# Kernel tuning notes

Measured on AMD Instinct MI355X. Metric: run time of the kernel, lower is better.

Reference implementation:

```python
import jax, jax.numpy as jnp
import numpy as np

MUL = 128          # multiplicity for every irrep
N = 100000         # number of nodes
INV_SQRT_FANIN = 1.0 / np.sqrt(MUL).astype(np.float32)


def setup_inputs() -> dict:
    key = jax.random.key(0)
    k = jax.random.split(key, 5)
    return {
        "x": jax.random.normal(k[0], (N, MUL + 3 * MUL), dtype=jnp.float32),   # [N, 512] = 128x0e + 128x1o
        "w1_s": jax.random.normal(k[1], (MUL, 2 * MUL), dtype=jnp.float32),    # 0e path of linear_1 (-> scalars+gates)
        "w1_v": jax.random.normal(k[2], (MUL, MUL), dtype=jnp.float32),        # 1o path of linear_1
        "w2_s": jax.random.normal(k[3], (MUL, MUL), dtype=jnp.float32),        # 0e path of linear_2
        "w2_v": jax.random.normal(k[4], (MUL, MUL), dtype=jnp.float32),        # 1o path of linear_2
    }


def reference(x, w1_s, w1_v, w2_s, w2_v):
    n = x.shape[0]
    x0 = x[:, :MUL]                              # [N, 128]  scalars (0e)
    x1 = x[:, MUL:].reshape(n, MUL, 3)           # [N, 128, 3] vectors (1o)

    # linear_1: 128x0e+128x1o -> 256x0e + 128x1o (scalars | gates | gated)
    s = (x0 @ w1_s) * INV_SQRT_FANIN             # [N, 256]
    v = jnp.einsum('nui,uv->nvi', x1, w1_v) * INV_SQRT_FANIN  # [N, 128, 3]

    # Gate: silu on scalars, silu(gates) broadcast-multiplies the vectors
    h0 = jax.nn.silu(s[:, :MUL])                 # [N, 128]
    g = jax.nn.silu(s[:, MUL:])                  # [N, 128]
    h1 = v * g[:, :, None]                       # [N, 128, 3]

    # linear_2: 128x0e+128x1o -> 128x0e+128x1o
    y0 = (h0 @ w2_s) * INV_SQRT_FANIN            # [N, 128]
    y1 = jnp.einsum('nui,uv->nvi', h1, w2_v) * INV_SQRT_FANIN  # [N, 128, 3]
    return jnp.concatenate([y0, y1.reshape(n, 3 * MUL)], axis=-1)  # [N, 512]
```

## Files before the change

### kernel.cpp

```cpp
#include <hip/hip_runtime.h>
#include <hip/hip_bf16.h>
#include <cstdint>

#define MUL   128
#define ROWS  32
#define NW    8
#define TPB   (NW * 64)

typedef __attribute__((ext_vector_type(8))) short  short8;
typedef __attribute__((ext_vector_type(8))) __bf16 bf16x8;
typedef __attribute__((ext_vector_type(4))) float  f32x4;
typedef __attribute__((ext_vector_type(4))) short  short4v;

__device__ __forceinline__ short f2bf(float f) {
    union { float f; unsigned int u; } v; v.f = f;
    unsigned int u = v.u;
    u += 0x7fffu + ((u >> 16) & 1u);
    return (short)(u >> 16);
}

__device__ __forceinline__ float silu_f(float x) {
    return x / (1.0f + __expf(-x));
}

#define RSB     256
#define OFF_X0  0
#define OFF_X1  8192
#define OFF_H0  32768
#define OFF_H1  40960
#define SMEM_BYTES 65536

__device__ __forceinline__ int swz(int row, int byteInRow) {
    return row * RSB + (byteInRow ^ ((row & 7) << 4));
}

__device__ __forceinline__ short8 lds_afrag(const char* sm, int off, int r0, int ks, int lane) {
    int row = r0 + (lane & 15);
    int bi  = ks * 64 + ((lane >> 4) << 4);
    return *(const short8*)(sm + off + swz(row, bi));
}

__device__ __forceinline__ short8 bfrag_f32(const float* __restrict__ W, int ldn,
                                            int c0, int ks, int lane) {
    const float* p = W + (size_t)(ks * 32 + ((lane >> 4) << 3)) * ldn + (c0 + (lane & 15));
    short8 r;
#pragma unroll
    for (int j = 0; j < 8; ++j) r[j] = f2bf(p[(size_t)j * ldn]);
    return r;
}

__device__ __forceinline__ f32x4 mfma16(short8 a, short8 b, f32x4 c) {
    return __builtin_amdgcn_mfma_f32_16x16x32_bf16(
        __builtin_bit_cast(bf16x8, a), __builtin_bit_cast(bf16x8, b), c, 0, 0, 0);
}

__global__ __launch_bounds__(TPB, 4) void gnlr_fused_kernel(
    const float* __restrict__ x,
    const float* __restrict__ w1s, const float* __restrict__ w1v,
    const float* __restrict__ w2s, const float* __restrict__ w2v,
    float* __restrict__ out, int n)
{
    __shared__ alignas(16) char sm[SMEM_BYTES];

    const int tid   = threadIdx.x;
    const int lane  = tid & 63;
    const int w     = tid >> 6;
    const int row0g = blockIdx.x * ROWS;
    const float INV = 0.08838834764831845f;

#pragma unroll
    for (int it = 0; it < 2; ++it) {
        int idx = tid + it * TPB;
        int row = idx >> 5;
        int c4  = (idx & 31) << 2;
        int rg  = row0g + row; if (rg >= n) rg = n - 1;
        float4 f = *(const float4*)(x + (size_t)rg * 512 + c4);
        short4v pk;
        pk.x = f2bf(f.x); pk.y = f2bf(f.y); pk.z = f2bf(f.z); pk.w = f2bf(f.w);
        *(short4v*)(sm + OFF_X0 + swz(row, c4 * 2)) = pk;
    }
#pragma unroll
    for (int it = 0; it < 2; ++it) {
        int idx = tid + it * TPB;
        int row = idx >> 5;
        int grp = idx & 31;
        int rg  = row0g + row; if (rg >= n) rg = n - 1;
        const float* p = x + (size_t)rg * 512 + 128 + grp * 12;
        float4 fa = *(const float4*)(p);
        float4 fb = *(const float4*)(p + 4);
        float4 fc = *(const float4*)(p + 8);
        float f[12] = { fa.x, fa.y, fa.z, fa.w, fb.x, fb.y, fb.z, fb.w, fc.x, fc.y, fc.z, fc.w };
#pragma unroll
        for (int i = 0; i < 3; ++i) {
            short4v pk;
            pk.x = f2bf(f[i]); pk.y = f2bf(f[3 + i]); pk.z = f2bf(f[6 + i]); pk.w = f2bf(f[9 + i]);
            *(short4v*)(sm + OFF_X1 + i * 8192 + swz(row, grp * 8)) = pk;
        }
    }
    __syncthreads();

    const f32x4 z = { 0.f, 0.f, 0.f, 0.f };
    const int c0 = w * 16;

    short8 bs0[4], bs1[4];
#pragma unroll
    for (int ks = 0; ks < 4; ++ks) {
        bs0[ks] = bfrag_f32(w1s, 256, c0, ks, lane);
        bs1[ks] = bfrag_f32(w1s, 256, 128 + c0, ks, lane);
    }
    float g_reg[2][4];
#pragma unroll
    for (int rt = 0; rt < 2; ++rt) {
        f32x4 a0 = z, a1 = z;
#pragma unroll
        for (int ks = 0; ks < 4; ++ks) {
            short8 a = lds_afrag(sm, OFF_X0, rt * 16, ks, lane);
            a0 = mfma16(a, bs0[ks], a0);
            a1 = mfma16(a, bs1[ks], a1);
        }
#pragma unroll
        for (int j = 0; j < 4; ++j) {
            int row = rt * 16 + ((lane >> 4) << 2) + j;
            int col = c0 + (lane & 15);
            float h0 = silu_f(a0[j] * INV);
            *(short*)(sm + OFF_H0 + swz(row, col * 2)) = f2bf(h0);
            g_reg[rt][j] = silu_f(a1[j] * INV);
        }
    }

    short8 bv[4];
#pragma unroll
    for (int ks = 0; ks < 4; ++ks) bv[ks] = bfrag_f32(w1v, 128, c0, ks, lane);
#pragma unroll
    for (int i = 0; i < 3; ++i) {
#pragma unroll
        for (int rt = 0; rt < 2; ++rt) {
            f32x4 acc = z;
#pragma unroll
            for (int ks = 0; ks < 4; ++ks) {
                short8 a = lds_afrag(sm, OFF_X1 + i * 8192, rt * 16, ks, lane);
                acc = mfma16(a, bv[ks], acc);
            }
#pragma unroll
            for (int j = 0; j < 4; ++j) {
                int row = rt * 16 + ((lane >> 4) << 2) + j;
                int col = c0 + (lane & 15);
                float h1 = acc[j] * INV * g_reg[rt][j];
                *(short*)(sm + OFF_H1 + i * 8192 + swz(row, col * 2)) = f2bf(h1);
            }
        }
    }
    __syncthreads();

    short8 b2s[4], b2v[4];
#pragma unroll
    for (int ks = 0; ks < 4; ++ks) {
        b2s[ks] = bfrag_f32(w2s, 128, c0, ks, lane);
        b2v[ks] = bfrag_f32(w2v, 128, c0, ks, lane);
    }
#pragma unroll
    for (int rt = 0; rt < 2; ++rt) {
        f32x4 acc = z;
#pragma unroll
        for (int ks = 0; ks < 4; ++ks)
            acc = mfma16(lds_afrag(sm, OFF_H0, rt * 16, ks, lane), b2s[ks], acc);
#pragma unroll
        for (int j = 0; j < 4; ++j) {
            int row = rt * 16 + ((lane >> 4) << 2) + j;
            int rg  = row0g + row;
            if (rg < n) out[(size_t)rg * 512 + c0 + (lane & 15)] = acc[j] * INV;
        }
    }
#pragma unroll
    for (int i = 0; i < 3; ++i) {
#pragma unroll
        for (int rt = 0; rt < 2; ++rt) {
            f32x4 acc = z;
#pragma unroll
            for (int ks = 0; ks < 4; ++ks)
                acc = mfma16(lds_afrag(sm, OFF_H1 + i * 8192, rt * 16, ks, lane), b2v[ks], acc);
#pragma unroll
            for (int j = 0; j < 4; ++j) {
                int row = rt * 16 + ((lane >> 4) << 2) + j;
                int rg  = row0g + row;
                if (rg < n) out[(size_t)rg * 512 + 128 + 3 * (c0 + (lane & 15)) + i] = acc[j] * INV;
            }
        }
    }
}

extern "C" void kernel_launch(void* const* d_in, const int* in_sizes, int n_in,
                              void* d_out, int out_size, void* d_ws, size_t ws_size,
                              hipStream_t stream) {
    const float* x   = (const float*)d_in[0];
    const float* w1s = (const float*)d_in[1];
    const float* w1v = (const float*)d_in[2];
    const float* w2s = (const float*)d_in[3];
    const float* w2v = (const float*)d_in[4];
    float* out = (float*)d_out;
    const int n = in_sizes[0] / (4 * MUL);
    const int grid = (n + ROWS - 1) / ROWS;
    gnlr_fused_kernel<<<grid, TPB, 0, stream>>>(x, w1s, w1v, w2s, w2v, out, n);
}
```

Before: 127.3 us.

## Prepack bf16 weight fragments, swap MFMA operands, reuse LDS, vectorize stores

A small prep kernel converts all four weight matrices once into bf16 MFMA fragment layout in workspace, so each block loads a packed fragment with one coalesced load instead of eight strided fp32 loads and conversions. The MFMA operands are swapped so each lane holds four consecutive columns of one row, which allows float4 output stores and interleaves the three vector components into contiguous stores. The gated-vector intermediate now overwrites the x0/x1 regions of shared memory, shrinking LDS to 40KB to allow 8 blocks per CU, at the cost of extra barriers per component. An extra kernel launch is added per call.

```diff
diff --git a/kernel.cpp b/kernel.cpp
--- a/kernel.cpp
+++ b/kernel.cpp
@@ -1,11 +1,8 @@
 #include <hip/hip_runtime.h>
-#include <hip/hip_bf16.h>
 #include <cstdint>
 
-#define MUL   128
-#define ROWS  32
-#define NW    8
-#define TPB   (NW * 64)
+#define TPB  512
+#define ROWS 32
 
 typedef __attribute__((ext_vector_type(8))) short  short8;
 typedef __attribute__((ext_vector_type(8))) __bf16 bf16x8;
@@ -18,35 +15,34 @@
     u += 0x7fffu + ((u >> 16) & 1u);
     return (short)(u >> 16);
 }
-
-__device__ __forceinline__ float silu_f(float x) {
-    return x / (1.0f + __expf(-x));
-}
-
-#define RSB     256
-#define OFF_X0  0
-#define OFF_X1  8192
-#define OFF_H0  32768
-#define OFF_H1  40960
-#define SMEM_BYTES 65536
-
-__device__ __forceinline__ int swz(int row, int byteInRow) {
-    return row * RSB + (byteInRow ^ ((row & 7) << 4));
-}
-
-__device__ __forceinline__ short8 lds_afrag(const char* sm, int off, int r0, int ks, int lane) {
+__device__ __forceinline__ float silu_f(float x) { return x / (1.0f + __expf(-x)); }
+
+#define RSB 256
+#define OFF_X0 0
+#define OFF_X1 8192
+#define OFF_H0 32768
+#define SMEM_BYTES 40960
+
+__device__ __forceinline__ int swz(int row, int b) { return row * RSB + (b ^ ((row & 7) << 4)); }
+
+__device__ __forceinline__ short8 lds_bfrag(const char* sm, int off, int r0, int ks, int lane) {
     int row = r0 + (lane & 15);
     int bi  = ks * 64 + ((lane >> 4) << 4);
     return *(const short8*)(sm + off + swz(row, bi));
 }
 
-__device__ __forceinline__ short8 bfrag_f32(const float* __restrict__ W, int ldn,
-                                            int c0, int ks, int lane) {
-    const float* p = W + (size_t)(ks * 32 + ((lane >> 4) << 3)) * ldn + (c0 + (lane & 15));
-    short8 r;
-#pragma unroll
-    for (int j = 0; j < 8; ++j) r[j] = f2bf(p[(size_t)j * ldn]);
-    return r;
+template<bool PACKED>
+__device__ __forceinline__ short8 wfrag(const short8* pw, const float* W, int ldn,
+                                        int gtile, int ltile, int ks, int lane) {
+    if constexpr (PACKED) {
+        return pw[(gtile * 4 + ks) * 64 + lane];
+    } else {
+        const float* p = W + (size_t)(ks * 32 + ((lane >> 4) << 3)) * ldn + ltile * 16 + (lane & 15);
+        short8 r;
+#pragma unroll
+        for (int j = 0; j < 8; ++j) r[j] = f2bf(p[(size_t)j * ldn]);
+        return r;
+    }
 }
 
 __device__ __forceinline__ f32x4 mfma16(short8 a, short8 b, f32x4 c) {
@@ -54,10 +50,30 @@
         __builtin_bit_cast(bf16x8, a), __builtin_bit_cast(bf16x8, b), c, 0, 0, 0);
 }
 
-__global__ __launch_bounds__(TPB, 4) void gnlr_fused_kernel(
+__global__ void prep_pack(const float* __restrict__ w1s, const float* __restrict__ w1v,
+                          const float* __restrict__ w2s, const float* __restrict__ w2v,
+                          short8* __restrict__ pk) {
+    int b = blockIdx.x;
+    int t = threadIdx.x;
+    int ks = t >> 6, lane = t & 63;
+    const float* W; int ldn, lt;
+    if (b < 16)      { W = w1s; ldn = 256; lt = b; }
+    else if (b < 24) { W = w1v; ldn = 128; lt = b - 16; }
+    else if (b < 32) { W = w2s; ldn = 128; lt = b - 24; }
+    else             { W = w2v; ldn = 128; lt = b - 32; }
+    const float* p = W + (size_t)(ks * 32 + ((lane >> 4) << 3)) * ldn + lt * 16 + (lane & 15);
+    short8 r;
+#pragma unroll
+    for (int j = 0; j < 8; ++j) r[j] = f2bf(p[(size_t)j * ldn]);
+    pk[(b * 4 + ks) * 64 + lane] = r;
+}
+
+template<bool PACKED>
+__global__ __launch_bounds__(TPB, 8) void gnlr_fused_kernel(
     const float* __restrict__ x,
     const float* __restrict__ w1s, const float* __restrict__ w1v,
     const float* __restrict__ w2s, const float* __restrict__ w2v,
+    const short8* __restrict__ pw,
     float* __restrict__ out, int n)
 {
     __shared__ alignas(16) char sm[SMEM_BYTES];
@@ -66,7 +82,9 @@
     const int lane  = tid & 63;
     const int w     = tid >> 6;
     const int row0g = blockIdx.x * ROWS;
+    const int c0    = w * 16;
     const float INV = 0.08838834764831845f;
+    const f32x4 z = { 0.f, 0.f, 0.f, 0.f };
 
 #pragma unroll
     for (int it = 0; it < 2; ++it) {
@@ -75,9 +93,9 @@
         int c4  = (idx & 31) << 2;
         int rg  = row0g + row; if (rg >= n) rg = n - 1;
         float4 f = *(const float4*)(x + (size_t)rg * 512 + c4);
-        short4v pk;
-        pk.x = f2bf(f.x); pk.y = f2bf(f.y); pk.z = f2bf(f.z); pk.w = f2bf(f.w);
-        *(short4v*)(sm + OFF_X0 + swz(row, c4 * 2)) = pk;
+        short4v pkv;
+        pkv.x = f2bf(f.x); pkv.y = f2bf(f.y); pkv.z = f2bf(f.z); pkv.w = f2bf(f.w);
+        *(short4v*)(sm + OFF_X0 + swz(row, c4 * 2)) = pkv;
     }
 #pragma unroll
     for (int it = 0; it < 2; ++it) {
@@ -92,98 +110,103 @@
         float f[12] = { fa.x, fa.y, fa.z, fa.w, fb.x, fb.y, fb.z, fb.w, fc.x, fc.y, fc.z, fc.w };
 #pragma unroll
         for (int i = 0; i < 3; ++i) {
-            short4v pk;
-            pk.x = f2bf(f[i]); pk.y = f2bf(f[3 + i]); pk.z = f2bf(f[6 + i]); pk.w = f2bf(f[9 + i]);
-            *(short4v*)(sm + OFF_X1 + i * 8192 + swz(row, grp * 8)) = pk;
+            short4v pkv;
+            pkv.x = f2bf(f[i]); pkv.y = f2bf(f[3 + i]); pkv.z = f2bf(f[6 + i]); pkv.w = f2bf(f[9 + i]);
+            *(short4v*)(sm + OFF_X1 + i * 8192 + swz(row, grp * 8)) = pkv;
         }
     }
     __syncthreads();
 
-    const f32x4 z = { 0.f, 0.f, 0.f, 0.f };
-    const int c0 = w * 16;
-
-    short8 bs0[4], bs1[4];
-#pragma unroll
-    for (int ks = 0; ks < 4; ++ks) {
-        bs0[ks] = bfrag_f32(w1s, 256, c0, ks, lane);
-        bs1[ks] = bfrag_f32(w1s, 256, 128 + c0, ks, lane);
-    }
     float g_reg[2][4];
-#pragma unroll
-    for (int rt = 0; rt < 2; ++rt) {
-        f32x4 a0 = z, a1 = z;
-#pragma unroll
-        for (int ks = 0; ks < 4; ++ks) {
-            short8 a = lds_afrag(sm, OFF_X0, rt * 16, ks, lane);
-            a0 = mfma16(a, bs0[ks], a0);
-            a1 = mfma16(a, bs1[ks], a1);
-        }
-#pragma unroll
-        for (int j = 0; j < 4; ++j) {
-            int row = rt * 16 + ((lane >> 4) << 2) + j;
-            int col = c0 + (lane & 15);
-            float h0 = silu_f(a0[j] * INV);
-            *(short*)(sm + OFF_H0 + swz(row, col * 2)) = f2bf(h0);
-            g_reg[rt][j] = silu_f(a1[j] * INV);
-        }
-    }
-
-    short8 bv[4];
-#pragma unroll
-    for (int ks = 0; ks < 4; ++ks) bv[ks] = bfrag_f32(w1v, 128, c0, ks, lane);
-#pragma unroll
-    for (int i = 0; i < 3; ++i) {
+    {
+        short8 bs[4];
+#pragma unroll
+        for (int ks = 0; ks < 4; ++ks) bs[ks] = wfrag<PACKED>(pw, w1s, 256, w, w, ks, lane);
 #pragma unroll
         for (int rt = 0; rt < 2; ++rt) {
             f32x4 acc = z;
 #pragma unroll
-            for (int ks = 0; ks < 4; ++ks) {
-                short8 a = lds_afrag(sm, OFF_X1 + i * 8192, rt * 16, ks, lane);
-                acc = mfma16(a, bv[ks], acc);
-            }
-#pragma unroll
-            for (int j = 0; j < 4; ++j) {
-                int row = rt * 16 + ((lane >> 4) << 2) + j;
-                int col = c0 + (lane & 15);
-                float h1 = acc[j] * INV * g_reg[rt][j];
-                *(short*)(sm + OFF_H1 + i * 8192 + swz(row, col * 2)) = f2bf(h1);
+            for (int ks = 0; ks < 4; ++ks)
+                acc = mfma16(bs[ks], lds_bfrag(sm, OFF_X0, rt * 16, ks, lane), acc);
+            short4v pkv;
+#pragma unroll
+            for (int j = 0; j < 4; ++j) pkv[j] = f2bf(silu_f(acc[j] * INV));
+            int row = rt * 16 + (lane & 15);
+            *(short4v*)(sm + OFF_H0 + swz(row, 2 * (c0 + ((lane >> 4) << 2)))) = pkv;
+        }
+#pragma unroll
+        for (int ks = 0; ks < 4; ++ks) bs[ks] = wfrag<PACKED>(pw, w1s, 256, 8 + w, 8 + w, ks, lane);
+#pragma unroll
+        for (int rt = 0; rt < 2; ++rt) {
+            f32x4 acc = z;
+#pragma unroll
+            for (int ks = 0; ks < 4; ++ks)
+                acc = mfma16(bs[ks], lds_bfrag(sm, OFF_X0, rt * 16, ks, lane), acc);
+#pragma unroll
+            for (int j = 0; j < 4; ++j) g_reg[rt][j] = silu_f(acc[j] * INV);
+        }
+    }
+
+    {
+        short8 bv[4];
+#pragma unroll
+        for (int ks = 0; ks < 4; ++ks) bv[ks] = wfrag<PACKED>(pw, w1v, 128, 16 + w, w, ks, lane);
+#pragma unroll
+        for (int i = 0; i < 3; ++i) {
+            __syncthreads();
+#pragma unroll
+            for (int rt = 0; rt < 2; ++rt) {
+                f32x4 acc = z;
+#pragma unroll
+                for (int ks = 0; ks < 4; ++ks)
+                    acc = mfma16(bv[ks], lds_bfrag(sm, OFF_X1 + i * 8192, rt * 16, ks, lane), acc);
+                short4v pkv;
+#pragma unroll
+                for (int j = 0; j < 4; ++j) pkv[j] = f2bf(acc[j] * INV * g_reg[rt][j]);
+                int row = rt * 16 + (lane & 15);
+                *(short4v*)(sm + i * 8192 + swz(row, 2 * (c0 + ((lane >> 4) << 2)))) = pkv;
             }
         }
     }
     __syncthreads();
 
-    short8 b2s[4], b2v[4];
-#pragma unroll
-    for (int ks = 0; ks < 4; ++ks) {
-        b2s[ks] = bfrag_f32(w2s, 128, c0, ks, lane);
-        b2v[ks] = bfrag_f32(w2v, 128, c0, ks, lane);
-    }
-#pragma unroll
-    for (int rt = 0; rt < 2; ++rt) {
-        f32x4 acc = z;
-#pragma unroll
-        for (int ks = 0; ks < 4; ++ks)
-            acc = mfma16(lds_afrag(sm, OFF_H0, rt * 16, ks, lane), b2s[ks], acc);
-#pragma unroll
-        for (int j = 0; j < 4; ++j) {
-            int row = rt * 16 + ((lane >> 4) << 2) + j;
-            int rg  = row0g + row;
-            if (rg < n) out[(size_t)rg * 512 + c0 + (lane & 15)] = acc[j] * INV;
-        }
-    }
-#pragma unroll
-    for (int i = 0; i < 3; ++i) {
+    {
+        short8 b2[4];
+#pragma unroll
+        for (int ks = 0; ks < 4; ++ks) b2[ks] = wfrag<PACKED>(pw, w2s, 128, 24 + w, w, ks, lane);
 #pragma unroll
         for (int rt = 0; rt < 2; ++rt) {
             f32x4 acc = z;
 #pragma unroll
             for (int ks = 0; ks < 4; ++ks)
-                acc = mfma16(lds_afrag(sm, OFF_H1 + i * 8192, rt * 16, ks, lane), b2v[ks], acc);
-#pragma unroll
-            for (int j = 0; j < 4; ++j) {
-                int row = rt * 16 + ((lane >> 4) << 2) + j;
-                int rg  = row0g + row;
-                if (rg < n) out[(size_t)rg * 512 + 128 + 3 * (c0 + (lane & 15)) + i] = acc[j] * INV;
+                acc = mfma16(b2[ks], lds_bfrag(sm, OFF_H0, rt * 16, ks, lane), acc);
+            int rg = row0g + rt * 16 + (lane & 15);
+            if (rg < n) {
+                float4 o = { acc[0] * INV, acc[1] * INV, acc[2] * INV, acc[3] * INV };
+                *(float4*)(out + (size_t)rg * 512 + c0 + ((lane >> 4) << 2)) = o;
+            }
+        }
+#pragma unroll
+        for (int ks = 0; ks < 4; ++ks) b2[ks] = wfrag<PACKED>(pw, w2v, 128, 32 + w, w, ks, lane);
+#pragma unroll
+        for (int rt = 0; rt < 2; ++rt) {
+            f32x4 a3[3];
+#pragma unroll
+            for (int i = 0; i < 3; ++i) {
+                a3[i] = z;
+#pragma unroll
+                for (int ks = 0; ks < 4; ++ks)
+                    a3[i] = mfma16(b2[ks], lds_bfrag(sm, i * 8192, rt * 16, ks, lane), a3[i]);
+            }
+            int rg = row0g + rt * 16 + (lane & 15);
+            if (rg < n) {
+                float* base = out + (size_t)rg * 512 + 128 + 3 * (c0 + ((lane >> 4) << 2));
+                float4 s0 = { a3[0][0] * INV, a3[1][0] * INV, a3[2][0] * INV, a3[0][1] * INV };
+                float4 s1 = { a3[1][1] * INV, a3[2][1] * INV, a3[0][2] * INV, a3[1][2] * INV };
+                float4 s2 = { a3[2][2] * INV, a3[0][3] * INV, a3[1][3] * INV, a3[2][3] * INV };
+                *(float4*)(base + 0) = s0;
+                *(float4*)(base + 4) = s1;
+                *(float4*)(base + 8) = s2;
             }
         }
     }
@@ -198,7 +221,15 @@
     const float* w2s = (const float*)d_in[3];
     const float* w2v = (const float*)d_in[4];
     float* out = (float*)d_out;
-    const int n = in_sizes[0] / (4 * MUL);
+    const int n = in_sizes[0] / 512;
     const int grid = (n + ROWS - 1) / ROWS;
-    gnlr_fused_kernel<<<grid, TPB, 0, stream>>>(x, w1s, w1v, w2s, w2v, out, n);
-}
+    const size_t need = (size_t)40 * 4 * 64 * sizeof(short8);
+    if (ws_size >= need) {
+        prep_pack<<<40, 256, 0, stream>>>(w1s, w1v, w2s, w2v, (short8*)d_ws);
+        gnlr_fused_kernel<true><<<grid, TPB, 0, stream>>>(x, w1s, w1v, w2s, w2v,
+                                                          (const short8*)d_ws, out, n);
+    } else {
+        gnlr_fused_kernel<false><<<grid, TPB, 0, stream>>>(x, w1s, w1v, w2s, w2v,
+                                                           nullptr, out, n);
+    }
+}
```

Result: faster. 107.5 us (-15.6%).
